# Kernel optimization log

Hardware: AMD Instinct MI355X
Metric: run time of the kernel (lower is better)

## Reference

```python
import jax, jax.numpy as jnp
import numpy as np
from jax import lax

FS = 48000.0
PI = 3.14159265358979323846

def bilinear_low_shelf(fc, gain_db, Q, fs):
    A = 10.0 ** (gain_db / 40.0)
    w0 = 2.0 * PI * fc / fs
    alpha = jnp.sin(w0) / (2.0 * Q)
    cosw = jnp.cos(w0)
    sqA = jnp.sqrt(A)
    b0 = A * (A + 1 - (A - 1) * cosw + 2 * sqA * alpha)
    b1 = 2 * A * (A - 1 - (A + 1) * cosw)
    b2 = A * (A + 1 - (A - 1) * cosw - 2 * sqA * alpha)
    a0 = A + 1 + (A - 1) * cosw + 2 * sqA * alpha
    a1 = -2 * (A - 1 + (A + 1) * cosw)
    a2 = A + 1 + (A - 1) * cosw - 2 * sqA * alpha
    return (b0 / a0, b1 / a0, b2 / a0, a1 / a0, a2 / a0)

def biquad(x, b0, b1, b2, a1, a2):
    # x: [B, T]; direct-form-II-transposed biquad with zero initial state
    B = x.shape[0]
    z0 = (jnp.zeros((B,), x.dtype), jnp.zeros((B,), x.dtype))
    def step(carry, xn):
        z1, z2 = carry
        yn = b0 * xn + z1
        z1n = b1 * xn - a1 * yn + z2
        z2n = b2 * xn - a2 * yn
        return (z1n, z2n), yn
    _, yT = lax.scan(step, z0, x.T)  # scan over time axis
    return yT.T

def setup_inputs() -> dict:
    key = jax.random.key(0)
    x = jax.random.normal(key, (64, 480000), dtype=jnp.float32)
    return {
        "x": x,
        "low_gain_db": jnp.float32(6.0),
        "mid_gain_db": jnp.float32(-3.0),
        "mid_fc": jnp.float32(800.0),
        "mid_Q": jnp.float32(1.0),
        "high_gain_db": jnp.float32(4.0),
    }

def reference(x, low_gain_db, mid_gain_db, mid_fc, mid_Q, high_gain_db):
    c = bilinear_low_shelf(jnp.float32(120.0), low_gain_db, jnp.float32(0.707), FS)
    y = biquad(x, *c)
    c = bilinear_low_shelf(mid_fc, mid_gain_db, mid_Q, FS)
    y = biquad(y, *c)
    c = bilinear_low_shelf(jnp.float32(4000.0), high_gain_db, jnp.float32(0.707), FS)
    y = biquad(y, *c)
    return y
```

## Files before the change

kernel.cpp:

```cpp
#include <hip/hip_runtime.h>
#include <math.h>


constexpr int T_LEN  = 480000;
constexpr int B_ROWS = 64;
constexpr int CHUNK  = 64;
constexpr int LOG2C  = 6;
constexpr int KCH    = T_LEN / CHUNK;
constexpr int NT     = 128;
constexpr int HISTC  = 12;
constexpr int MTERM  = 12;
constexpr int OUTC   = NT - HISTC;
constexpr int BLKROW = (KCH + OUTC - 1) / OUTC;
constexpr int NBLK   = B_ROWS * BLKROW;

struct Coeffs { float b0, b1, b2, a1, a2; };

__device__ __forceinline__ float rfl(float v) {
    return __int_as_float(__builtin_amdgcn_readfirstlane(__float_as_int(v)));
}

__device__ __forceinline__ Coeffs shelf(float fc, float gdb, float Q) {
    float A  = powf(10.0f, gdb * (1.0f / 40.0f));
    float w0 = 2.0f * 3.14159265358979323846f * fc / 48000.0f;
    float sw = sinf(w0), cw = cosf(w0);
    float alpha = sw / (2.0f * Q);
    float sqA = sqrtf(A);
    float b0 = A * ((A + 1.0f) - (A - 1.0f) * cw + 2.0f * sqA * alpha);
    float b1 = 2.0f * A * ((A - 1.0f) - (A + 1.0f) * cw);
    float b2 = A * ((A + 1.0f) - (A - 1.0f) * cw - 2.0f * sqA * alpha);
    float a0 = (A + 1.0f) + (A - 1.0f) * cw + 2.0f * sqA * alpha;
    float a1 = -2.0f * ((A - 1.0f) + (A + 1.0f) * cw);
    float a2 = (A + 1.0f) + (A - 1.0f) * cw - 2.0f * sqA * alpha;
    float rr = 1.0f / a0;
    Coeffs c;
    c.b0 = rfl(b0 * rr); c.b1 = rfl(b1 * rr); c.b2 = rfl(b2 * rr);
    c.a1 = rfl(a1 * rr); c.a2 = rfl(a2 * rr);
    return c;
}

__device__ __forceinline__ float bq(float xn, const Coeffs& c, float& z1, float& z2) {
    float y = fmaf(c.b0, xn, z1);
    z1 = fmaf(-c.a1, y, fmaf(c.b1, xn, z2));
    z2 = fmaf(c.b2, xn, -(c.a2 * y));
    return y;
}

__device__ __forceinline__ float step6(float s[6], float x,
                                       const Coeffs& c1, const Coeffs& c2, const Coeffs& c3) {
    float y1 = bq(x,  c1, s[0], s[1]);
    float y2 = bq(y1, c2, s[2], s[3]);
    float y3 = bq(y2, c3, s[4], s[5]);
    return y3;
}

__device__ __forceinline__ float corr(float y0, const float* cnp, const float t6[6]) {
    float4 ca = *(const float4*)(cnp);
    float2 cb = *(const float2*)(cnp + 4);
    float acc = fmaf(ca.x, t6[0], y0);
    acc = fmaf(ca.y, t6[1], acc);
    acc = fmaf(ca.z, t6[2], acc);
    acc = fmaf(ca.w, t6[3], acc);
    acc = fmaf(cb.x, t6[4], acc);
    acc = fmaf(cb.y, t6[5], acc);
    return acc;
}

__global__ __launch_bounds__(128, 4) void k_fused(
    const float* __restrict__ x,
    const float* __restrict__ p_lg, const float* __restrict__ p_mg,
    const float* __restrict__ p_mf, const float* __restrict__ p_mq,
    const float* __restrict__ p_hg,
    float* __restrict__ out)
{
    __shared__ __align__(16) float smem[2048];
    __shared__ float M[36];
    __shared__ float Pw[LOG2C * 36];
    __shared__ float Crow[8];
    __shared__ __align__(16) float cn[64 * 8];

    const int t    = threadIdx.x;
    const int lane = t & 63;
    const int w    = t >> 6;
    const int r = blockIdx.x / BLKROW;
    const int b = blockIdx.x - r * BLKROW;
    const int c = b * OUTC + t - HISTC;
    const int cbase = b * OUTC - HISTC;
    const bool active = (c >= 0) && (c < KCH);

    Coeffs c1 = shelf(120.0f,  *p_lg, 0.707f);
    Coeffs c2 = shelf(*p_mf,   *p_mg, *p_mq);
    Coeffs c3 = shelf(4000.0f, *p_hg, 0.707f);

    float4 xv[16];
    {
        int cc = c < 0 ? 0 : (c >= KCH ? KCH - 1 : c);
        const float4* lp = (const float4*)(x + (long long)r * T_LEN + (long long)cc * CHUNK);
        if (active) {
            #pragma unroll
            for (int q = 0; q < 16; ++q) xv[q] = lp[q];
        } else {
            #pragma unroll
            for (int q = 0; q < 16; ++q) xv[q] = make_float4(0.f, 0.f, 0.f, 0.f);
        }
    }

    if (w == 0) {
        const int i  = lane / 6;
        const int j  = lane - 6 * i;
        const int i6 = i * 6;
        float e[6];
        #pragma unroll
        for (int jj = 0; jj < 6; ++jj) e[jj] = (jj == j) ? 1.0f : 0.0f;
        float y = step6(e, 0.0f, c1, c2, c3);
        if (lane < 6) Crow[lane] = y;
        float aM = e[0];
        #pragma unroll
        for (int ii = 1; ii < 6; ++ii) aM = (i == ii) ? e[ii] : aM;
        for (int it = 0; it < LOG2C; ++it) {
            if (lane < 36) Pw[it * 36 + lane] = aM;
            float acc = 0.f;
            #pragma unroll
            for (int q = 0; q < 6; ++q) {
                int sA = i6 + q; if (sA > 63) sA = 63;
                acc = fmaf(__shfl(aM, sA, 64), __shfl(aM, q * 6 + j, 64), acc);
            }
            aM = acc;
        }
        if (lane < 36) M[lane] = aM;
    }

    float s[6] = {0.f, 0.f, 0.f, 0.f, 0.f, 0.f};
    #pragma unroll
    for (int q = 0; q < 16; ++q) {
        float4 v = xv[q];
        v.x = step6(s, v.x, c1, c2, c3);
        v.y = step6(s, v.y, c1, c2, c3);
        v.z = step6(s, v.z, c1, c2, c3);
        v.w = step6(s, v.w, c1, c2, c3);
        xv[q] = v;
    }
    #pragma unroll
    for (int i = 0; i < 6; ++i) smem[t * 7 + i] = s[i];

    __syncthreads();

    float a[36];
    #pragma unroll
    for (int i = 0; i < 36; ++i) a[i] = rfl(M[i]);

    if (w == 1) {
        float row[6];
        #pragma unroll
        for (int jj = 0; jj < 6; ++jj) row[jj] = Crow[jj];
        #pragma unroll
        for (int k = 0; k < LOG2C; ++k) {
            if ((lane >> k) & 1) {
                const float* P = Pw + k * 36;
                float nr[6];
                #pragma unroll
                for (int jj = 0; jj < 6; ++jj) {
                    float acc = 0.f;
                    #pragma unroll
                    for (int q = 0; q < 6; ++q) acc = fmaf(row[q], P[q * 6 + jj], acc);
                    nr[jj] = acc;
                }
                #pragma unroll
                for (int jj = 0; jj < 6; ++jj) row[jj] = nr[jj];
            }
        }
        #pragma unroll
        for (int jj = 0; jj < 6; ++jj) cn[lane * 8 + jj] = row[jj];
    }

    float t6[6] = {0.f, 0.f, 0.f, 0.f, 0.f, 0.f};
    int m0 = t - MTERM; if (m0 < 0) m0 = 0;
    for (int m = m0; m < t; ++m) {
        float dm[6];
        #pragma unroll
        for (int i = 0; i < 6; ++i) dm[i] = smem[m * 7 + i];
        float nt6[6];
        #pragma unroll
        for (int i = 0; i < 6; ++i) {
            float acc = dm[i];
            #pragma unroll
            for (int j = 0; j < 6; ++j) acc = fmaf(a[i * 6 + j], t6[j], acc);
            nt6[i] = acc;
        }
        #pragma unroll
        for (int i = 0; i < 6; ++i) t6[i] = nt6[i];
    }

    __syncthreads();

    #pragma unroll
    for (int q = 0; q < 16; ++q) {
        float4 v = xv[q];
        v.x = corr(v.x, cn + (4 * q + 0) * 8, t6);
        v.y = corr(v.y, cn + (4 * q + 1) * 8, t6);
        v.z = corr(v.z, cn + (4 * q + 2) * 8, t6);
        v.w = corr(v.w, cn + (4 * q + 3) * 8, t6);
        xv[q] = v;
    }

    float4* qv = ((float4*)smem) + w * 256;
    float4* op = (float4*)(out + (long long)r * T_LEN);
    #pragma unroll
    for (int j = 0; j < 4; ++j) {
        if ((lane >> 4) == j) {
            const int sl  = lane & 15;
            const int key = sl & 7;
            #pragma unroll
            for (int q = 0; q < 16; ++q)
                qv[sl * 16 + (q ^ key)] = xv[q];
        }
        const long long base4 = (long long)(cbase + w * 64 + 16 * j) * 16;
        #pragma unroll
        for (int i = 0; i < 4; ++i) {
            const int sl = i * 4 + (lane >> 4);
            const int qq = lane & 15;
            const int tr = w * 64 + 16 * j + sl;
            const int cc = cbase + tr;
            if (tr >= HISTC && cc < KCH) {
                op[base4 + i * 64 + lane] = qv[sl * 16 + (qq ^ (sl & 7))];
            }
        }
    }
}

extern "C" void kernel_launch(void* const* d_in, const int* in_sizes, int n_in,
                              void* d_out, int out_size, void* d_ws, size_t ws_size,
                              hipStream_t stream) {
    const float* x  = (const float*)d_in[0];
    const float* lg = (const float*)d_in[1];
    const float* mg = (const float*)d_in[2];
    const float* mf = (const float*)d_in[3];
    const float* mq = (const float*)d_in[4];
    const float* hg = (const float*)d_in[5];
    float* out = (float*)d_out;

    hipLaunchKernelGGL(k_fused, dim3(NBLK), dim3(NT), 0, stream,
                       x, lg, mg, mf, mq, hg, out);
}
```

Baseline: 234.6 us.

## Split per-thread chunk scan into two independent half-chunk recurrences for ILP

Each thread now runs two 32-sample zero-state biquad-cascade recurrences in an interleaved fashion instead of one 64-sample serial chain. The goal is to halve the dependency-chain length and raise instruction-level parallelism. The half-chunk states are combined using the precomputed 32-step transition power, and the second half gets a separate correction vector. The cost is extra 6x6 matrix-vector work, an additional barrier, and more register pressure.

```diff
diff --git a/kernel.cpp b/kernel.cpp
--- a/kernel.cpp
+++ b/kernel.cpp
@@ -54,15 +54,15 @@
     return y3;
 }
 
-__device__ __forceinline__ float corr(float y0, const float* cnp, const float t6[6]) {
+__device__ __forceinline__ float corr(float y0, const float* cnp, const float v6[6]) {
     float4 ca = *(const float4*)(cnp);
     float2 cb = *(const float2*)(cnp + 4);
-    float acc = fmaf(ca.x, t6[0], y0);
-    acc = fmaf(ca.y, t6[1], acc);
-    acc = fmaf(ca.z, t6[2], acc);
-    acc = fmaf(ca.w, t6[3], acc);
-    acc = fmaf(cb.x, t6[4], acc);
-    acc = fmaf(cb.y, t6[5], acc);
+    float acc = fmaf(ca.x, v6[0], y0);
+    acc = fmaf(ca.y, v6[1], acc);
+    acc = fmaf(ca.z, v6[2], acc);
+    acc = fmaf(ca.w, v6[3], acc);
+    acc = fmaf(cb.x, v6[4], acc);
+    acc = fmaf(cb.y, v6[5], acc);
     return acc;
 }
 
@@ -77,7 +77,7 @@
     __shared__ float M[36];
     __shared__ float Pw[LOG2C * 36];
     __shared__ float Crow[8];
-    __shared__ __align__(16) float cn[64 * 8];
+    __shared__ __align__(16) float cn[32 * 8];
 
     const int t    = threadIdx.x;
     const int lane = t & 63;
@@ -130,31 +130,48 @@
         if (lane < 36) M[lane] = aM;
     }
 
-    float s[6] = {0.f, 0.f, 0.f, 0.f, 0.f, 0.f};
-    #pragma unroll
-    for (int q = 0; q < 16; ++q) {
-        float4 v = xv[q];
-        v.x = step6(s, v.x, c1, c2, c3);
-        v.y = step6(s, v.y, c1, c2, c3);
-        v.z = step6(s, v.z, c1, c2, c3);
-        v.w = step6(s, v.w, c1, c2, c3);
-        xv[q] = v;
-    }
-    #pragma unroll
-    for (int i = 0; i < 6; ++i) smem[t * 7 + i] = s[i];
+    float s1[6] = {0.f, 0.f, 0.f, 0.f, 0.f, 0.f};
+    float s2[6] = {0.f, 0.f, 0.f, 0.f, 0.f, 0.f};
+    #pragma unroll
+    for (int q = 0; q < 8; ++q) {
+        float4 va = xv[q];
+        float4 vb = xv[q + 8];
+        va.x = step6(s1, va.x, c1, c2, c3);  vb.x = step6(s2, vb.x, c1, c2, c3);
+        va.y = step6(s1, va.y, c1, c2, c3);  vb.y = step6(s2, vb.y, c1, c2, c3);
+        va.z = step6(s1, va.z, c1, c2, c3);  vb.z = step6(s2, vb.z, c1, c2, c3);
+        va.w = step6(s1, va.w, c1, c2, c3);  vb.w = step6(s2, vb.w, c1, c2, c3);
+        xv[q] = va;
+        xv[q + 8] = vb;
+    }
 
     __syncthreads();
 
+    const float* A32 = Pw + 5 * 36;
+    {
+        float dt[6];
+        #pragma unroll
+        for (int i = 0; i < 6; ++i) {
+            float acc = s2[i];
+            #pragma unroll
+            for (int j = 0; j < 6; ++j) acc = fmaf(A32[i * 6 + j], s1[j], acc);
+            dt[i] = acc;
+        }
+        #pragma unroll
+        for (int i = 0; i < 6; ++i) smem[t * 7 + i] = dt[i];
+    }
+
+    __syncthreads();
+
     float a[36];
     #pragma unroll
     for (int i = 0; i < 36; ++i) a[i] = rfl(M[i]);
 
-    if (w == 1) {
+    if (w == 1 && lane < 32) {
         float row[6];
         #pragma unroll
         for (int jj = 0; jj < 6; ++jj) row[jj] = Crow[jj];
         #pragma unroll
-        for (int k = 0; k < LOG2C; ++k) {
+        for (int k = 0; k < 5; ++k) {
             if ((lane >> k) & 1) {
                 const float* P = Pw + k * 36;
                 float nr[6];
@@ -193,14 +210,29 @@
 
     __syncthreads();
 
-    #pragma unroll
-    for (int q = 0; q < 16; ++q) {
-        float4 v = xv[q];
-        v.x = corr(v.x, cn + (4 * q + 0) * 8, t6);
-        v.y = corr(v.y, cn + (4 * q + 1) * 8, t6);
-        v.z = corr(v.z, cn + (4 * q + 2) * 8, t6);
-        v.w = corr(v.w, cn + (4 * q + 3) * 8, t6);
-        xv[q] = v;
+    float u[6];
+    #pragma unroll
+    for (int i = 0; i < 6; ++i) {
+        float acc = s1[i];
+        #pragma unroll
+        for (int j = 0; j < 6; ++j) acc = fmaf(A32[i * 6 + j], t6[j], acc);
+        u[i] = acc;
+    }
+
+    #pragma unroll
+    for (int q = 0; q < 8; ++q) {
+        float4 va = xv[q];
+        va.x = corr(va.x, cn + (4 * q + 0) * 8, t6);
+        va.y = corr(va.y, cn + (4 * q + 1) * 8, t6);
+        va.z = corr(va.z, cn + (4 * q + 2) * 8, t6);
+        va.w = corr(va.w, cn + (4 * q + 3) * 8, t6);
+        xv[q] = va;
+        float4 vb = xv[q + 8];
+        vb.x = corr(vb.x, cn + (4 * q + 0) * 8, u);
+        vb.y = corr(vb.y, cn + (4 * q + 1) * 8, u);
+        vb.z = corr(vb.z, cn + (4 * q + 2) * 8, u);
+        vb.w = corr(vb.w, cn + (4 * q + 3) * 8, u);
+        xv[q + 8] = vb;
     }
 
     float4* qv = ((float4*)smem) + w * 256;
```

Result: no change. 235.8 us (+0.5%).
